# Optimization experiments

Measured on AMD Instinct MI355X. Metric: run time of the kernel, lower is better.

## Reference

```python
import jax, jax.numpy as jnp
import numpy as np

N_ATOMS = 100000
N_EDGES = 800000
ATOM_FDIM = 133
HIDDEN = 256
DEPTH = 3
NUM_MOLS = 4096
BN_EPS = 1e-5


def setup_inputs() -> dict:
    key = jax.random.key(0)
    ks = jax.random.split(key, 16)
    f_atoms = jax.random.normal(ks[0], (N_ATOMS, ATOM_FDIM), dtype=jnp.float32)
    edge_index = jax.random.randint(ks[1], (2, N_EDGES), 0, N_ATOMS, dtype=jnp.int64)
    segment_ids = jnp.sort(jax.random.randint(ks[2], (N_ATOMS,), 0, NUM_MOLS, dtype=jnp.int64))
    s = 1.0 / np.sqrt(HIDDEN)
    return {
        "f_atoms": f_atoms,
        "W_in_w": jax.random.normal(ks[3], (ATOM_FDIM, HIDDEN), dtype=jnp.float32) / np.sqrt(ATOM_FDIM),
        "W_in_b": jnp.zeros((HIDDEN,), dtype=jnp.float32),
        "w1": jax.random.normal(ks[4], (DEPTH, HIDDEN, HIDDEN), dtype=jnp.float32) * s,
        "b1": jnp.zeros((DEPTH, HIDDEN), dtype=jnp.float32),
        "g1": jnp.ones((DEPTH, HIDDEN), dtype=jnp.float32),
        "be1": jnp.zeros((DEPTH, HIDDEN), dtype=jnp.float32),
        "w2": jax.random.normal(ks[5], (DEPTH, HIDDEN, HIDDEN), dtype=jnp.float32) * s,
        "b2": jnp.zeros((DEPTH, HIDDEN), dtype=jnp.float32),
        "g2": jnp.ones((DEPTH, HIDDEN), dtype=jnp.float32),
        "be2": jnp.zeros((DEPTH, HIDDEN), dtype=jnp.float32),
        "eps": jnp.zeros((DEPTH,), dtype=jnp.float32),
        "edge_index": edge_index,
        "segment_ids": segment_ids,
    }


def batchnorm(h, gamma, beta):
    # BatchNorm1d with batch statistics over the node dimension (training-mode math)
    mean = jnp.mean(h, axis=0)
    var = jnp.var(h, axis=0)
    return (h - mean) * jax.lax.rsqrt(var + BN_EPS) * gamma + beta


def reference(f_atoms, W_in_w, W_in_b, w1, b1, g1, be1, w2, b2, g2, be2, eps,
              edge_index, segment_ids):
    src, dst = edge_index[0], edge_index[1]
    x = jax.nn.relu(f_atoms @ W_in_w + W_in_b)  # [N, H]
    for i in range(DEPTH):
        agg = jnp.zeros_like(x).at[dst].add(x[src])  # gather + scatter-add
        h = agg + (1.0 + eps[i]) * x                 # epsilon self-term
        h = jax.nn.relu(batchnorm(h @ w1[i] + b1[i], g1[i], be1[i]))
        h = jax.nn.relu(batchnorm(h @ w2[i] + b2[i], g2[i], be2[i]))
        x = h  # dropout = identity (eval)
    sums = jax.ops.segment_sum(x, segment_ids, num_segments=NUM_MOLS)
    counts = jax.ops.segment_sum(jnp.ones((x.shape[0],), x.dtype), segment_ids,
                                 num_segments=NUM_MOLS)
    return sums / jnp.maximum(counts, 1.0)[:, None]  # per-molecule mean
```

## Files before the change

### kernel.cpp

```cpp
#include <hip/hip_runtime.h>
#include <hip/hip_bf16.h>

#define NA 100000
#define NE 800000
#define FDIM 133
#define KIN 192
#define H 256
#define NMOL 4096

typedef __attribute__((ext_vector_type(8))) short s16x8;
typedef __attribute__((ext_vector_type(4))) float f32x4;
typedef __attribute__((ext_vector_type(4))) unsigned short u16x4;

__device__ __forceinline__ float bf2f(unsigned short h) {
    unsigned u = ((unsigned)h) << 16;
    return __builtin_bit_cast(float, u);
}
__device__ __forceinline__ unsigned short f2bf(float f) {
    unsigned u = __builtin_bit_cast(unsigned, f);
    u = u + 0x7FFFu + ((u >> 16) & 1u);
    return (unsigned short)(u >> 16);
}

__device__ __forceinline__ int swz(int row, int g) {
    return row * 64 + ((g ^ (row & 7)) << 3);
}

template<bool A_F32, bool AFFINE, bool RELU_OUT, bool STATS>
__global__ __launch_bounds__(256) void gemm_k(
    const void* __restrict__ Avoid,
    const unsigned short* __restrict__ BT,
    const float* __restrict__ bias,
    const float* __restrict__ aSc, const float* __restrict__ aSh,
    unsigned short* __restrict__ C,
    float* __restrict__ stSum, float* __restrict__ stSq,
    int M, int Kpad)
{
    __shared__ short lsA[128 * 64];
    __shared__ short lsB[128 * 64];
    __shared__ float lsSc[256], lsSh[256];
    __shared__ float lsS[128], lsQ[128];

    const int t = threadIdx.x;
    const int m0 = blockIdx.y * 128;
    const int n0 = blockIdx.x * 128;

    if (STATS && t < 128) { lsS[t] = 0.f; lsQ[t] = 0.f; }
    if (AFFINE) { lsSc[t] = aSc[t]; lsSh[t] = aSh[t]; }
    if (AFFINE) __syncthreads();

    const int sr = t >> 3;
    const int sg = t & 7;
    const int lane = t & 63;
    const int wid = t >> 6;
    const int wm = wid >> 1, wn = wid & 1;
    const int fr = lane & 15, fg = lane >> 4;

    f32x4 acc[4][4];
    #pragma unroll
    for (int i = 0; i < 4; i++)
        #pragma unroll
        for (int j = 0; j < 4; j++)
            acc[i][j] = f32x4{0.f, 0.f, 0.f, 0.f};

    const int nK = Kpad >> 6;
    s16x8 ra[4], rb[4];

    auto loadRegs = [&](int kc) {
        const int k0 = kc * 64;
        #pragma unroll
        for (int p = 0; p < 4; ++p) {
            int r = p * 32 + sr;
            int ga = m0 + r;
            if (A_F32) {
                const float* Af = (const float*)Avoid;
                s16x8 v;
                #pragma unroll
                for (int e = 0; e < 8; ++e) {
                    int k = k0 + sg * 8 + e;
                    float f = (ga < M && k < FDIM) ? Af[(size_t)ga * FDIM + k] : 0.f;
                    v[e] = (short)f2bf(f);
                }
                ra[p] = v;
            } else {
                const unsigned short* A = (const unsigned short*)Avoid;
                s16x8 z = {0,0,0,0,0,0,0,0};
                ra[p] = (ga < M) ? *(const s16x8*)(A + (size_t)ga * Kpad + k0 + sg * 8) : z;
            }
            rb[p] = *(const s16x8*)(BT + (size_t)(n0 + p * 32 + sr) * Kpad + k0 + sg * 8);
        }
    };
    auto writeLds = [&](int kc) {
        const int k0 = kc * 64;
        #pragma unroll
        for (int p = 0; p < 4; ++p) {
            int r = p * 32 + sr;
            s16x8 va = ra[p];
            if (AFFINE) {
                #pragma unroll
                for (int e = 0; e < 8; ++e) {
                    int k = k0 + sg * 8 + e;
                    float f = bf2f((unsigned short)va[e]);
                    f = fmaxf(f * lsSc[k] + lsSh[k], 0.f);
                    va[e] = (short)f2bf(f);
                }
            }
            *(s16x8*)&lsA[swz(r, sg)] = va;
            *(s16x8*)&lsB[swz(r, sg)] = rb[p];
        }
    };

    loadRegs(0);
    for (int kc = 0; kc < nK; ++kc) {
        writeLds(kc);
        __syncthreads();
        if (kc + 1 < nK) loadRegs(kc + 1);
        #pragma unroll
        for (int ks = 0; ks < 2; ++ks) {
            s16x8 af[4], bg[4];
            #pragma unroll
            for (int mi = 0; mi < 4; ++mi)
                af[mi] = *(const s16x8*)&lsA[swz(wm * 64 + mi * 16 + fr, ks * 4 + fg)];
            #pragma unroll
            for (int ni = 0; ni < 4; ++ni)
                bg[ni] = *(const s16x8*)&lsB[swz(wn * 64 + ni * 16 + fr, ks * 4 + fg)];
            #pragma unroll
            for (int mi = 0; mi < 4; ++mi)
                #pragma unroll
                for (int ni = 0; ni < 4; ++ni)
                    acc[mi][ni] = __builtin_amdgcn_mfma_f32_16x16x32_bf16(
                        af[mi], bg[ni], acc[mi][ni], 0, 0, 0);
        }
        __syncthreads();
    }

    float bc[4];
    #pragma unroll
    for (int ni = 0; ni < 4; ++ni)
        bc[ni] = bias[n0 + wn * 64 + ni * 16 + fr];
    float cs[4] = {0.f, 0.f, 0.f, 0.f}, cq[4] = {0.f, 0.f, 0.f, 0.f};
    #pragma unroll
    for (int mi = 0; mi < 4; ++mi) {
        #pragma unroll
        for (int r = 0; r < 4; ++r) {
            int row = m0 + wm * 64 + mi * 16 + fg * 4 + r;
            if (row < M) {
                #pragma unroll
                for (int ni = 0; ni < 4; ++ni) {
                    float v = acc[mi][ni][r] + bc[ni];
                    if (RELU_OUT) v = fmaxf(v, 0.f);
                    if (STATS) { cs[ni] += v; cq[ni] += v * v; }
                    C[(size_t)row * H + n0 + wn * 64 + ni * 16 + fr] = f2bf(v);
                }
            }
        }
    }
    if (STATS) {
        #pragma unroll
        for (int ni = 0; ni < 4; ++ni) {
            atomicAdd(&lsS[wn * 64 + ni * 16 + fr], cs[ni]);
            atomicAdd(&lsQ[wn * 64 + ni * 16 + fr], cq[ni]);
        }
        __syncthreads();
        if (t < 128) {
            atomicAdd(&stSum[n0 + t], lsS[t]);
            atomicAdd(&stSq[n0 + t], lsQ[t]);
        }
    }
}

__global__ void bnfin_k(float* __restrict__ sum, float* __restrict__ sumsq,
                        const float* __restrict__ g, const float* __restrict__ be,
                        float* __restrict__ scOut, float* __restrict__ shOut) {
    int c = threadIdx.x;
    float mean = sum[c] * (1.0f / NA);
    float var = sumsq[c] * (1.0f / NA) - mean * mean;
    float sc = g[c] * rsqrtf(var + 1e-5f);
    scOut[c] = sc;
    shOut[c] = be[c] - mean * sc;
    sum[c] = 0.f; sumsq[c] = 0.f;
}

__global__ void zero_k(int* __restrict__ counts, float* __restrict__ st) {
    int i = blockIdx.x * 256 + threadIdx.x;
    if (i < NA) counts[i] = 0;
    if (blockIdx.x == 0 && threadIdx.x < 256) { st[threadIdx.x] = 0.f; st[threadIdx.x + 256] = 0.f; }
}

__global__ void hist_k(const int* __restrict__ dst, int* __restrict__ counts) {
    int e = blockIdx.x * 256 + threadIdx.x;
    if (e < NE) atomicAdd(&counts[dst[e]], 1);
}
__global__ void scan1_k(const int* __restrict__ counts, int* __restrict__ excl, int* __restrict__ bsum) {
    __shared__ int sd[256];
    int i = blockIdx.x * 256 + threadIdx.x;
    int c = (i < NA) ? counts[i] : 0;
    sd[threadIdx.x] = c;
    __syncthreads();
    for (int off = 1; off < 256; off <<= 1) {
        int v = (threadIdx.x >= off) ? sd[threadIdx.x - off] : 0;
        __syncthreads();
        sd[threadIdx.x] += v;
        __syncthreads();
    }
    if (i < NA) excl[i] = sd[threadIdx.x] - c;
    if (threadIdx.x == 255) bsum[blockIdx.x] = sd[255];
}
__global__ void scan2_k(int* __restrict__ bsum, int nb) {
    __shared__ int sd[512];
    int t = threadIdx.x;
    int v = (t < nb) ? bsum[t] : 0;
    sd[t] = v;
    __syncthreads();
    for (int off = 1; off < 512; off <<= 1) {
        int u = (t >= off) ? sd[t - off] : 0;
        __syncthreads();
        sd[t] += u;
        __syncthreads();
    }
    if (t < nb) bsum[t] = sd[t] - v;
}
__global__ void scan3_k(int* __restrict__ rowstart, const int* __restrict__ bsum, int* __restrict__ cursor) {
    int i = blockIdx.x * 256 + threadIdx.x;
    if (i < NA) {
        int v = rowstart[i] + bsum[blockIdx.x];
        rowstart[i] = v;
        cursor[i] = v;
    }
}
__global__ void fill_k(const int* __restrict__ src, const int* __restrict__ dstArr,
                       int* __restrict__ cursor, int* __restrict__ esrc) {
    int e = blockIdx.x * 256 + threadIdx.x;
    if (e < NE) {
        int d = dstArr[e];
        int pos = atomicAdd(&cursor[d], 1);
        esrc[pos] = src[e];
    }
}

template<bool AFF>
__global__ __launch_bounds__(256) void agg_k(const unsigned short* __restrict__ X,
    const float* __restrict__ sc, const float* __restrict__ sh,
    const int* __restrict__ rowstart, const int* __restrict__ counts,
    const int* __restrict__ esrc, const float* __restrict__ epsArr, int layer,
    unsigned short* __restrict__ AGG)
{
    int wid = threadIdx.x >> 6, lane = threadIdx.x & 63;
    int row = blockIdx.x * 4 + wid;
    if (row >= NA) return;
    int half = lane >> 5;
    int c0 = (lane & 31) * 8;

    float s8[8], h8[8];
    if (AFF) {
        f32x4 a = *(const f32x4*)(sc + c0), b = *(const f32x4*)(sc + c0 + 4);
        f32x4 c = *(const f32x4*)(sh + c0), d = *(const f32x4*)(sh + c0 + 4);
        #pragma unroll
        for (int e = 0; e < 4; e++) { s8[e] = a[e]; s8[e + 4] = b[e]; h8[e] = c[e]; h8[e + 4] = d[e]; }
    }

    float a0[8] = {0,0,0,0,0,0,0,0}, a1[8] = {0,0,0,0,0,0,0,0};
    auto gath = [&](int i, float* a) {
        int sr2 = esrc[i];
        s16x8 u = *(const s16x8*)(X + (size_t)sr2 * H + c0);
        #pragma unroll
        for (int e = 0; e < 8; e++) {
            float f = bf2f((unsigned short)u[e]);
            if (AFF) f = fmaxf(f * s8[e] + h8[e], 0.f);
            a[e] += f;
        }
    };

    int s = rowstart[row], eEnd = s + counts[row];
    int i = s + half;
    for (; i + 2 < eEnd; i += 4) { gath(i, a0); gath(i + 2, a1); }
    if (i < eEnd) gath(i, a0);

    if (half == 0) {
        float e1 = 1.0f + epsArr[layer];
        s16x8 u = *(const s16x8*)(X + (size_t)row * H + c0);
        #pragma unroll
        for (int e = 0; e < 8; e++) {
            float f = bf2f((unsigned short)u[e]);
            if (AFF) f = fmaxf(f * s8[e] + h8[e], 0.f);
            a0[e] += f * e1;
        }
    }

    s16x8 o;
    #pragma unroll
    for (int e = 0; e < 8; e++) {
        float tot = a0[e] + a1[e];
        tot += __shfl_xor(tot, 32);
        o[e] = (short)f2bf(tot);
    }
    if (half == 0)
        *(s16x8*)(AGG + (size_t)row * H + c0) = o;
}

__global__ void prep_all_k(const float* __restrict__ Win, const float* __restrict__ w1,
                           const float* __restrict__ w2, unsigned short* __restrict__ BTall) {
    int i = blockIdx.x * 256 + threadIdx.x;
    const int NIN = 256 * KIN;
    if (i < NIN) {
        int n = i / KIN, k = i % KIN;
        BTall[i] = (k < FDIM) ? f2bf(Win[(size_t)k * 256 + n]) : (unsigned short)0;
    } else if (i < NIN + 6 * 65536) {
        int j = i - NIN;
        int d = j >> 16, r = j & 65535;
        int n = r >> 8, k = r & 255;
        const float* W = (d & 1) ? w2 : w1;
        BTall[i] = f2bf(W[(size_t)(d >> 1) * 65536 + (size_t)k * 256 + n]);
    }
}

__global__ void molstart_k(const int* __restrict__ seg, int* __restrict__ ms) {
    int m = blockIdx.x * 256 + threadIdx.x;
    if (m <= NMOL) {
        int lo = 0, hi = NA;
        while (lo < hi) { int mid = (lo + hi) >> 1; if (seg[mid] < m) lo = mid + 1; else hi = mid; }
        ms[m] = lo;
    }
}
__global__ __launch_bounds__(64) void mean_k(const unsigned short* __restrict__ X,
    const float* __restrict__ sc, const float* __restrict__ sh,
    const int* __restrict__ ms, float* __restrict__ out)
{
    int m = blockIdx.x, lane = threadIdx.x;
    int c0 = lane * 4;
    f32x4 s4 = *(const f32x4*)(sc + c0);
    f32x4 h4 = *(const f32x4*)(sh + c0);
    int a = ms[m], b = ms[m + 1];
    f32x4 acc{0.f, 0.f, 0.f, 0.f};
    for (int r = a; r < b; ++r) {
        u16x4 u = *(const u16x4*)(X + (size_t)r * H + c0);
        #pragma unroll
        for (int e = 0; e < 4; e++) acc[e] += fmaxf(bf2f(u[e]) * s4[e] + h4[e], 0.f);
    }
    float inv = (b > a) ? 1.0f / (float)(b - a) : 0.0f;
    #pragma unroll
    for (int e = 0; e < 4; e++) acc[e] *= inv;
    *(f32x4*)(out + (size_t)m * H + c0) = acc;
}

extern "C" void kernel_launch(void* const* d_in, const int* in_sizes, int n_in,
                              void* d_out, int out_size, void* d_ws, size_t ws_size,
                              hipStream_t stream) {
    const float* f_atoms = (const float*)d_in[0];
    const float* W_in_w  = (const float*)d_in[1];
    const float* W_in_b  = (const float*)d_in[2];
    const float* w1  = (const float*)d_in[3];
    const float* b1  = (const float*)d_in[4];
    const float* g1  = (const float*)d_in[5];
    const float* be1 = (const float*)d_in[6];
    const float* w2  = (const float*)d_in[7];
    const float* b2  = (const float*)d_in[8];
    const float* g2  = (const float*)d_in[9];
    const float* be2 = (const float*)d_in[10];
    const float* epsArr = (const float*)d_in[11];
    const int* edge = (const int*)d_in[12];
    const int* seg  = (const int*)d_in[13];
    float* out = (float*)d_out;

    char* w = (char*)d_ws;
    size_t off = 0;
    auto alloc = [&](size_t bytes) {
        char* p = w + off;
        off = (off + bytes + 255) & ~(size_t)255;
        return p;
    };
    unsigned short* X   = (unsigned short*)alloc((size_t)NA * H * 2);
    unsigned short* AGG = (unsigned short*)alloc((size_t)NA * H * 2);
    unsigned short* T1  = (unsigned short*)alloc((size_t)NA * H * 2);
    unsigned short* BTall = (unsigned short*)alloc(((size_t)256 * KIN + 6 * 65536) * 2);
    float* stSum = (float*)alloc(256 * 4);
    float* stSq  = (float*)alloc(256 * 4);
    float* sc1 = (float*)alloc(256 * 4);
    float* sh1 = (float*)alloc(256 * 4);
    float* sc2 = (float*)alloc(256 * 4);
    float* sh2 = (float*)alloc(256 * 4);
    int* counts   = (int*)alloc((size_t)NA * 4);
    int* rowstart = (int*)alloc((size_t)NA * 4);
    int* cursor   = (int*)alloc((size_t)NA * 4);
    int* esrc     = (int*)alloc((size_t)NE * 4);
    int* bsum     = (int*)alloc(512 * 4);
    int* ms       = (int*)alloc((NMOL + 1) * 4);

    unsigned short* BTin = BTall;
    unsigned short* BT1[3], *BT2[3];
    for (int d = 0; d < 3; ++d) {
        BT1[d] = BTall + 256 * KIN + (size_t)(2 * d) * 65536;
        BT2[d] = BTall + 256 * KIN + (size_t)(2 * d + 1) * 65536;
    }

    const int* esrcIn = edge;
    const int* edst   = edge + NE;

    zero_k<<<(NA + 255) / 256, 256, 0, stream>>>(counts, stSum);
    prep_all_k<<<(256 * KIN + 6 * 65536 + 255) / 256, 256, 0, stream>>>(W_in_w, w1, w2, BTall);

    hist_k<<<(NE + 255) / 256, 256, 0, stream>>>(edst, counts);
    scan1_k<<<391, 256, 0, stream>>>(counts, rowstart, bsum);
    scan2_k<<<1, 512, 0, stream>>>(bsum, 391);
    scan3_k<<<391, 256, 0, stream>>>(rowstart, bsum, cursor);
    fill_k<<<(NE + 255) / 256, 256, 0, stream>>>(esrcIn, edst, cursor, esrc);
    molstart_k<<<(NMOL + 256) / 256, 256, 0, stream>>>(seg, ms);

    gemm_k<true, false, true, false><<<dim3(2, (NA + 127) / 128), 256, 0, stream>>>(
        f_atoms, BTin, W_in_b, nullptr, nullptr, X, nullptr, nullptr, NA, KIN);

    for (int d = 0; d < 3; ++d) {
        if (d == 0)
            agg_k<false><<<(NA + 3) / 4, 256, 0, stream>>>(X, nullptr, nullptr,
                rowstart, counts, esrc, epsArr, d, AGG);
        else
            agg_k<true><<<(NA + 3) / 4, 256, 0, stream>>>(X, sc2, sh2,
                rowstart, counts, esrc, epsArr, d, AGG);
        gemm_k<false, false, false, true><<<dim3(2, (NA + 127) / 128), 256, 0, stream>>>(
            AGG, BT1[d], b1 + d * 256, nullptr, nullptr, T1, stSum, stSq, NA, 256);
        bnfin_k<<<1, 256, 0, stream>>>(stSum, stSq, g1 + d * 256, be1 + d * 256, sc1, sh1);
        gemm_k<false, true, false, true><<<dim3(2, (NA + 127) / 128), 256, 0, stream>>>(
            T1, BT2[d], b2 + d * 256, sc1, sh1, X, stSum, stSq, NA, 256);
        bnfin_k<<<1, 256, 0, stream>>>(stSum, stSq, g2 + d * 256, be2 + d * 256, sc2, sh2);
    }

    mean_k<<<NMOL, 64, 0, stream>>>(X, sc2, sh2, ms, out);
}
```

Baseline: 736.0 us.

## Unroll edge gathers 4-wide, use CSR end pointer, widen mean pooling loads

The aggregation kernel now reads the row end from rowstart[row+1], stored as a sentinel, instead of a separate counts array. It splits each row's edges into two contiguous halves, one per half-wave, and issues four independent neighbor loads per iteration to raise memory-level parallelism. The mean-pooling kernel switches to 8-wide loads with two half-waves striding rows and a cross-lane shuffle reduction. The GEMM epilogue is restructured per column to cut live registers. Removing the row bound check relies on NA being divisible by 4.

```diff
diff --git a/kernel.cpp b/kernel.cpp
--- a/kernel.cpp
+++ b/kernel.cpp
@@ -10,7 +10,6 @@
 
 typedef __attribute__((ext_vector_type(8))) short s16x8;
 typedef __attribute__((ext_vector_type(4))) float f32x4;
-typedef __attribute__((ext_vector_type(4))) unsigned short u16x4;
 
 __device__ __forceinline__ float bf2f(unsigned short h) {
     unsigned u = ((unsigned)h) << 16;
@@ -87,7 +86,7 @@
                 s16x8 z = {0,0,0,0,0,0,0,0};
                 ra[p] = (ga < M) ? *(const s16x8*)(A + (size_t)ga * Kpad + k0 + sg * 8) : z;
             }
-            rb[p] = *(const s16x8*)(BT + (size_t)(n0 + p * 32 + sr) * Kpad + k0 + sg * 8);
+            rb[p] = *(const s16x8*)(BT + (size_t)(n0 + r) * Kpad + k0 + sg * 8);
         }
     };
     auto writeLds = [&](int kc) {
@@ -134,33 +133,30 @@
         __syncthreads();
     }
 
-    float bc[4];
     #pragma unroll
-    for (int ni = 0; ni < 4; ++ni)
-        bc[ni] = bias[n0 + wn * 64 + ni * 16 + fr];
-    float cs[4] = {0.f, 0.f, 0.f, 0.f}, cq[4] = {0.f, 0.f, 0.f, 0.f};
-    #pragma unroll
-    for (int mi = 0; mi < 4; ++mi) {
-        #pragma unroll
-        for (int r = 0; r < 4; ++r) {
-            int row = m0 + wm * 64 + mi * 16 + fg * 4 + r;
-            if (row < M) {
-                #pragma unroll
-                for (int ni = 0; ni < 4; ++ni) {
-                    float v = acc[mi][ni][r] + bc[ni];
+    for (int ni = 0; ni < 4; ++ni) {
+        int lcol = wn * 64 + ni * 16 + fr;
+        float bc = bias[n0 + lcol];
+        float cs = 0.f, cq = 0.f;
+        #pragma unroll
+        for (int mi = 0; mi < 4; ++mi) {
+            #pragma unroll
+            for (int r = 0; r < 4; ++r) {
+                int row = m0 + wm * 64 + mi * 16 + fg * 4 + r;
+                if (row < M) {
+                    float v = acc[mi][ni][r] + bc;
                     if (RELU_OUT) v = fmaxf(v, 0.f);
-                    if (STATS) { cs[ni] += v; cq[ni] += v * v; }
-                    C[(size_t)row * H + n0 + wn * 64 + ni * 16 + fr] = f2bf(v);
+                    if (STATS) { cs += v; cq += v * v; }
+                    C[(size_t)row * H + n0 + lcol] = f2bf(v);
                 }
             }
         }
+        if (STATS) {
+            atomicAdd(&lsS[lcol], cs);
+            atomicAdd(&lsQ[lcol], cq);
+        }
     }
     if (STATS) {
-        #pragma unroll
-        for (int ni = 0; ni < 4; ++ni) {
-            atomicAdd(&lsS[wn * 64 + ni * 16 + fr], cs[ni]);
-            atomicAdd(&lsQ[wn * 64 + ni * 16 + fr], cq[ni]);
-        }
         __syncthreads();
         if (t < 128) {
             atomicAdd(&stSum[n0 + t], lsS[t]);
@@ -181,10 +177,13 @@
     sum[c] = 0.f; sumsq[c] = 0.f;
 }
 
-__global__ void zero_k(int* __restrict__ counts, float* __restrict__ st) {
+__global__ void zero_k(int* __restrict__ counts, float* __restrict__ st, int* __restrict__ rowstart) {
     int i = blockIdx.x * 256 + threadIdx.x;
     if (i < NA) counts[i] = 0;
-    if (blockIdx.x == 0 && threadIdx.x < 256) { st[threadIdx.x] = 0.f; st[threadIdx.x + 256] = 0.f; }
+    if (blockIdx.x == 0) {
+        st[threadIdx.x] = 0.f; st[threadIdx.x + 256] = 0.f;
+        if (threadIdx.x == 0) rowstart[NA] = NE;
+    }
 }
 
 __global__ void hist_k(const int* __restrict__ dst, int* __restrict__ counts) {
@@ -241,13 +240,12 @@
 template<bool AFF>
 __global__ __launch_bounds__(256) void agg_k(const unsigned short* __restrict__ X,
     const float* __restrict__ sc, const float* __restrict__ sh,
-    const int* __restrict__ rowstart, const int* __restrict__ counts,
+    const int* __restrict__ rowstart,
     const int* __restrict__ esrc, const float* __restrict__ epsArr, int layer,
     unsigned short* __restrict__ AGG)
 {
     int wid = threadIdx.x >> 6, lane = threadIdx.x & 63;
     int row = blockIdx.x * 4 + wid;
-    if (row >= NA) return;
     int half = lane >> 5;
     int c0 = (lane & 31) * 8;
 
@@ -260,9 +258,7 @@
     }
 
     float a0[8] = {0,0,0,0,0,0,0,0}, a1[8] = {0,0,0,0,0,0,0,0};
-    auto gath = [&](int i, float* a) {
-        int sr2 = esrc[i];
-        s16x8 u = *(const s16x8*)(X + (size_t)sr2 * H + c0);
+    auto addv = [&](s16x8 u, float* a) {
         #pragma unroll
         for (int e = 0; e < 8; e++) {
             float f = bf2f((unsigned short)u[e]);
@@ -271,10 +267,23 @@
         }
     };
 
-    int s = rowstart[row], eEnd = s + counts[row];
-    int i = s + half;
-    for (; i + 2 < eEnd; i += 4) { gath(i, a0); gath(i + 2, a1); }
-    if (i < eEnd) gath(i, a0);
+    int s = rowstart[row], eEnd = rowstart[row + 1];
+    int cnt = eEnd - s, mid = s + (cnt >> 1);
+    int i = half ? mid : s;
+    int end = half ? eEnd : mid;
+    for (; i + 3 < end; i += 4) {
+        int e0 = esrc[i], e1 = esrc[i + 1], e2 = esrc[i + 2], e3 = esrc[i + 3];
+        s16x8 u0 = *(const s16x8*)(X + (size_t)e0 * H + c0);
+        s16x8 u1 = *(const s16x8*)(X + (size_t)e1 * H + c0);
+        s16x8 u2 = *(const s16x8*)(X + (size_t)e2 * H + c0);
+        s16x8 u3 = *(const s16x8*)(X + (size_t)e3 * H + c0);
+        addv(u0, a0); addv(u1, a1); addv(u2, a0); addv(u3, a1);
+    }
+    for (; i < end; ++i) {
+        int e0 = esrc[i];
+        s16x8 u = *(const s16x8*)(X + (size_t)e0 * H + c0);
+        addv(u, a0);
+    }
 
     if (half == 0) {
         float e1 = 1.0f + epsArr[layer];
@@ -327,20 +336,35 @@
     const int* __restrict__ ms, float* __restrict__ out)
 {
     int m = blockIdx.x, lane = threadIdx.x;
-    int c0 = lane * 4;
-    f32x4 s4 = *(const f32x4*)(sc + c0);
-    f32x4 h4 = *(const f32x4*)(sh + c0);
+    int half = lane >> 5;
+    int c0 = (lane & 31) * 8;
+    float s8[8], h8[8];
+    {
+        f32x4 a = *(const f32x4*)(sc + c0), b = *(const f32x4*)(sc + c0 + 4);
+        f32x4 c = *(const f32x4*)(sh + c0), d = *(const f32x4*)(sh + c0 + 4);
+        #pragma unroll
+        for (int e = 0; e < 4; e++) { s8[e] = a[e]; s8[e + 4] = b[e]; h8[e] = c[e]; h8[e + 4] = d[e]; }
+    }
     int a = ms[m], b = ms[m + 1];
-    f32x4 acc{0.f, 0.f, 0.f, 0.f};
-    for (int r = a; r < b; ++r) {
-        u16x4 u = *(const u16x4*)(X + (size_t)r * H + c0);
-        #pragma unroll
-        for (int e = 0; e < 4; e++) acc[e] += fmaxf(bf2f(u[e]) * s4[e] + h4[e], 0.f);
+    float acc[8] = {0,0,0,0,0,0,0,0};
+    for (int r = a + half; r < b; r += 2) {
+        s16x8 u = *(const s16x8*)(X + (size_t)r * H + c0);
+        #pragma unroll
+        for (int e = 0; e < 8; e++)
+            acc[e] += fmaxf(bf2f((unsigned short)u[e]) * s8[e] + h8[e], 0.f);
     }
     float inv = (b > a) ? 1.0f / (float)(b - a) : 0.0f;
+    f32x4 o0, o1;
     #pragma unroll
-    for (int e = 0; e < 4; e++) acc[e] *= inv;
-    *(f32x4*)(out + (size_t)m * H + c0) = acc;
+    for (int e = 0; e < 8; e++) {
+        float tot = acc[e] + __shfl_xor(acc[e], 32);
+        tot *= inv;
+        if (e < 4) o0[e] = tot; else o1[e - 4] = tot;
+    }
+    if (half == 0) {
+        *(f32x4*)(out + (size_t)m * H + c0) = o0;
+        *(f32x4*)(out + (size_t)m * H + c0 + 4) = o1;
+    }
 }
 
 extern "C" void kernel_launch(void* const* d_in, const int* in_sizes, int n_in,
@@ -380,7 +404,7 @@
     float* sc2 = (float*)alloc(256 * 4);
     float* sh2 = (float*)alloc(256 * 4);
     int* counts   = (int*)alloc((size_t)NA * 4);
-    int* rowstart = (int*)alloc((size_t)NA * 4);
+    int* rowstart = (int*)alloc((size_t)(NA + 1) * 4);
     int* cursor   = (int*)alloc((size_t)NA * 4);
     int* esrc     = (int*)alloc((size_t)NE * 4);
     int* bsum     = (int*)alloc(512 * 4);
@@ -396,7 +420,7 @@
     const int* esrcIn = edge;
     const int* edst   = edge + NE;
 
-    zero_k<<<(NA + 255) / 256, 256, 0, stream>>>(counts, stSum);
+    zero_k<<<(NA + 255) / 256, 256, 0, stream>>>(counts, stSum, rowstart);
     prep_all_k<<<(256 * KIN + 6 * 65536 + 255) / 256, 256, 0, stream>>>(W_in_w, w1, w2, BTall);
 
     hist_k<<<(NE + 255) / 256, 256, 0, stream>>>(edst, counts);
@@ -411,11 +435,11 @@
 
     for (int d = 0; d < 3; ++d) {
         if (d == 0)
-            agg_k<false><<<(NA + 3) / 4, 256, 0, stream>>>(X, nullptr, nullptr,
-                rowstart, counts, esrc, epsArr, d, AGG);
+            agg_k<false><<<NA / 4, 256, 0, stream>>>(X, nullptr, nullptr,
+                rowstart, esrc, epsArr, d, AGG);
         else
-            agg_k<true><<<(NA + 3) / 4, 256, 0, stream>>>(X, sc2, sh2,
-                rowstart, counts, esrc, epsArr, d, AGG);
+            agg_k<true><<<NA / 4, 256, 0, stream>>>(X, sc2, sh2,
+                rowstart, esrc, epsArr, d, AGG);
         gemm_k<false, false, false, true><<<dim3(2, (NA + 127) / 128), 256, 0, stream>>>(
             AGG, BT1[d], b1 + d * 256, nullptr, nullptr, T1, stSum, stSq, NA, 256);
         bnfin_k<<<1, 256, 0, stream>>>(stSum, stSq, g1 + d * 256, be1 + d * 256, sc1, sh1);
```

Result: slower. 785.4 us (+6.7%).
